# Performance work log

Hardware: AMD Instinct MI355X
Metric: run time of the kernel (lower is better)

Reference implementation:

```python
import jax, jax.numpy as jnp
import numpy as np

FP8_MAX = 448.0  # max normal of float8_e4m3fn
NUM_HEADS = 16


def act_quant(x):
    # per-tensor fp8 quantization: scale so max|x| maps to FP8_MAX
    scale = jnp.max(jnp.abs(x)) / FP8_MAX
    q = (x / scale).astype(jnp.float8_e4m3fn)
    return q, scale


def setup_inputs() -> dict:
    key = jax.random.key(0)
    k1, k2, k3, k4 = jax.random.split(key, 4)
    B, S, H = 2, 2048, 2048
    x = jax.random.normal(k1, (B, S, H), dtype=jnp.float32)
    W_qkv = jax.random.normal(k2, (H, 3 * H), dtype=jnp.float32) * (1.0 / np.sqrt(H))
    W_out = jax.random.normal(k3, (H, H), dtype=jnp.float32) * (1.0 / np.sqrt(H))
    b_out = jnp.zeros((H,), dtype=jnp.float32)
    return {"x": x, "W_qkv": W_qkv, "W_out": W_out, "b_out": b_out}


def reference(x, W_qkv, W_out, b_out):
    B, S, H = x.shape
    nH = NUM_HEADS
    hd = H // nH  # 128, matches head_dim default used for scaling

    qkv = jnp.einsum('bsh,hf->bsf', x, W_qkv)          # [B,S,3H]
    qkv = qkv.reshape(B, S, 3, nH, hd)
    q = qkv[:, :, 0].transpose(0, 2, 1, 3)             # [B,nH,S,hd]
    k = qkv[:, :, 1].transpose(0, 2, 1, 3)
    v = qkv[:, :, 2].transpose(0, 2, 1, 3)

    q8, q_scale = act_quant(q)
    k8, k_scale = act_quant(k)
    # fp8_gemm_optimized: dequantized GEMM = (a @ b) * a_scale * b_scale
    scores = jnp.einsum('bhqd,bhkd->bhqk',
                        q8.astype(jnp.float32), k8.astype(jnp.float32))
    scores = scores * (q_scale * k_scale) / jnp.sqrt(jnp.float32(hd))

    attn = jax.nn.softmax(scores, axis=-1)             # [B,nH,S,S]
    # (dropout omitted: deterministic / eval mode)

    v8, v_scale = act_quant(v)
    out = jnp.einsum('bhqk,bhkd->bhqd', attn, v8.astype(jnp.float32))
    out = out * v_scale                                # a_scale = 1 for attn weights

    out = out.transpose(0, 2, 1, 3).reshape(B, S, H)
    return jnp.einsum('bsh,ho->bso', out, W_out) + b_out
```

## Files before the change

kernel.cpp:

```cpp
#include <hip/hip_runtime.h>
#include <hip/hip_bf16.h>
#include <math.h>

#define B_   2
#define S_   2048
#define H_   2048
#define NH   16
#define HD   128
#define ROWS (B_ * S_)
#define F3   (3 * H_)
#define KS   2048
#define NKC  192

typedef _Float16 f16x8 __attribute__((ext_vector_type(8)));
typedef float    f32x4  __attribute__((ext_vector_type(4)));
typedef float    f32x16 __attribute__((ext_vector_type(16)));

union H2 { unsigned u; _Float16 h[2]; };
union H4 { ushort4 s4; _Float16 h[4]; };
union PU { unsigned u[4]; f16x8 v8; };

struct FragSet { f16x8 a[4]; f16x8 b[4]; };

__device__ __forceinline__ void gl_lds16(const void* g, void* l) {
  __builtin_amdgcn_global_load_lds(
      (const __attribute__((address_space(1))) void*)g,
      (__attribute__((address_space(3))) void*)l, 16, 0, 0);
}

__device__ __forceinline__ float quant_e4m3(float x) {
  float ax = fabsf(x);
  float q;
  if (ax < 0.015625f) {
    q = rintf(ax * 512.0f) * (1.0f / 512.0f);
  } else {
    unsigned eb = __float_as_uint(ax) & 0x7f800000u;
    float quantum = __uint_as_float(eb - (3u << 23));
    q = rintf(ax / quantum) * quantum;
    if (q > 448.0f) q = 448.0f;
  }
  return copysignf(q, x);
}

__global__ __launch_bounds__(256) void split_ab(
    const float* __restrict__ in, _Float16* __restrict__ hi,
    _Float16* __restrict__ lo) {
  const size_t i = (size_t)blockIdx.x * 256 + threadIdx.x;
  float4 v = ((const float4*)in)[i];
  H4 h, l;
  h.h[0] = (_Float16)v.x; l.h[0] = (_Float16)(v.x - (float)h.h[0]);
  h.h[1] = (_Float16)v.y; l.h[1] = (_Float16)(v.y - (float)h.h[1]);
  h.h[2] = (_Float16)v.z; l.h[2] = (_Float16)(v.z - (float)h.h[2]);
  h.h[3] = (_Float16)v.w; l.h[3] = (_Float16)(v.w - (float)h.h[3]);
  ((ushort4*)hi)[i] = h.s4;
  ((ushort4*)lo)[i] = l.s4;
}

__global__ __launch_bounds__(256) void split_tr(
    const float* __restrict__ in, _Float16* __restrict__ hi,
    _Float16* __restrict__ lo, int K, int N) {
  __shared__ _Float16 ht[64][72];
  __shared__ _Float16 lt[64][72];
  const int t = threadIdx.x;
  const int n0 = blockIdx.x * 64, k0 = blockIdx.y * 64;
#pragma unroll
  for (int p = 0; p < 4; p++) {
    const int k = p * 16 + (t >> 4);
    const int n = (t & 15) * 4;
    float4 v = *(const float4*)(in + (size_t)(k0 + k) * N + n0 + n);
    _Float16 h0 = (_Float16)v.x, h1 = (_Float16)v.y,
             h2 = (_Float16)v.z, h3 = (_Float16)v.w;
    ht[n + 0][k] = h0; lt[n + 0][k] = (_Float16)(v.x - (float)h0);
    ht[n + 1][k] = h1; lt[n + 1][k] = (_Float16)(v.y - (float)h1);
    ht[n + 2][k] = h2; lt[n + 2][k] = (_Float16)(v.z - (float)h2);
    ht[n + 3][k] = h3; lt[n + 3][k] = (_Float16)(v.w - (float)h3);
  }
  __syncthreads();
#pragma unroll
  for (int it = 0; it < 2; it++) {
    const int idx = it * 256 + t;
    const int r = idx >> 3, c = (idx & 7) * 8;
    *(uint4*)(hi + (size_t)(n0 + r) * K + k0 + c) = *(const uint4*)&ht[r][c];
    *(uint4*)(lo + (size_t)(n0 + r) * K + k0 + c) = *(const uint4*)&lt[r][c];
  }
}

#define ABUF(i) (lds + (i) * 12288)

#define STAGE32(tt, dstA) do {                                                 \
    const _Float16* As_ = ((tt) < 128) ? Ahi : Alo;                            \
    const _Float16* Bs_ = ((((tt) >> 6)) == 1) ? Btlo : Bthi;                  \
    const int koff_ = ((tt) & 63) << 5;                                        \
    {                                                                          \
      const int c0_ = t, r0_ = c0_ >> 2, cl0_ = c0_ & 3;                       \
      gl_lds16(As_ + (size_t)(row0 + r0_) * KS + koff_ + ((cl0_ ^ (r0_ & 3)) << 3), \
               (dstA) + c0_ * 8);                                              \
      const int c1_ = 512 + t, r1_ = c1_ >> 2, cl1_ = c1_ & 3;                 \
      gl_lds16(As_ + (size_t)(row0 + r1_) * KS + koff_ + ((cl1_ ^ (r1_ & 3)) << 3), \
               (dstA) + c1_ * 8);                                              \
      const int cb_ = t, rb_ = cb_ >> 2, clb_ = cb_ & 3;                       \
      gl_lds16(Bs_ + (size_t)(col0 + rb_) * KS + koff_ + ((clb_ ^ (rb_ & 3)) << 3), \
               (dstA) + 8192 + cb_ * 8);                                       \
    }                                                                          \
  } while (0)

#define READ_FRAGS(bi, FR) do {                                                \
    const _Float16* Ab_ = ABUF(bi);                                            \
    const _Float16* Bb_ = Ab_ + 8192;                                          \
    _Pragma("unroll")                                                          \
    for (int i_ = 0; i_ < 4; i_++) {                                           \
      const int r_ = wm * 64 + i_ * 16 + l15;                                  \
      (FR).a[i_] = *(const f16x8*)(Ab_ + r_ * 32 + ((g ^ (r_ & 3)) << 3));     \
    }                                                                          \
    _Pragma("unroll")                                                          \
    for (int j_ = 0; j_ < 4; j_++) {                                           \
      const int r_ = wn * 64 + j_ * 16 + l15;                                  \
      (FR).b[j_] = *(const f16x8*)(Bb_ + r_ * 32 + ((g ^ (r_ & 3)) << 3));     \
    }                                                                          \
  } while (0)

#define MFMA16(FR) do {                                                        \
    _Pragma("unroll")                                                          \
    for (int i_ = 0; i_ < 4; i_++)                                             \
      _Pragma("unroll")                                                        \
      for (int j_ = 0; j_ < 4; j_++)                                           \
        acc[i_][j_] = __builtin_amdgcn_mfma_f32_16x16x32_f16(                  \
            (FR).a[i_], (FR).b[j_], acc[i_][j_], 0, 0, 0);                     \
  } while (0)

#define BODY(u, kcv, FRc, FRn) do {                                            \
    const int kc_ = (kcv);                                                     \
    if (kc_ + 3 < NKC) STAGE32(kc_ + 3, ABUF(((u) + 3) & 3));                  \
    if (kc_ + 1 < NKC) READ_FRAGS(((u) + 1) & 3, FRn);                         \
    MFMA16(FRc);                                                               \
    if (kc_ < NKC - 3) { asm volatile("s_waitcnt vmcnt(3)" ::: "memory"); }    \
    else               { asm volatile("s_waitcnt vmcnt(0)" ::: "memory"); }    \
    __builtin_amdgcn_s_barrier();                                              \
  } while (0)

__global__ __launch_bounds__(512, 2) void gemm_split256(
    const _Float16* __restrict__ Ahi, const _Float16* __restrict__ Alo,
    const _Float16* __restrict__ Bthi, const _Float16* __restrict__ Btlo,
    float* __restrict__ C, const float* __restrict__ bias,
    unsigned* mx, int N, int has_bias) {
  __shared__ __align__(16) _Float16 lds[49152];
  const int t = threadIdx.x;
  const int wave = t >> 6, lane = t & 63;
  const int l15 = lane & 15, g = lane >> 4;
  const int wm = wave >> 1, wn = wave & 1;

  const int gx = gridDim.x;
  const int nwg = gx * gridDim.y;
  const int bid = blockIdx.y * gx + blockIdx.x;
  const int tile = (bid & 7) * (nwg >> 3) + (bid >> 3);
  const int row0 = (tile / gx) * 256, col0 = (tile % gx) * 128;

  f32x4 acc[4][4] = {};
  FragSet fr0, fr1;

  STAGE32(0, ABUF(0));
  STAGE32(1, ABUF(1));
  STAGE32(2, ABUF(2));
  asm volatile("s_waitcnt vmcnt(3)" ::: "memory");
  __builtin_amdgcn_s_barrier();
  READ_FRAGS(0, fr0);

  for (int grp = 0; grp < NKC / 4; grp++) {
    const int base = grp * 4;
    BODY(0, base + 0, fr0, fr1);
    BODY(1, base + 1, fr1, fr0);
    BODY(2, base + 2, fr0, fr1);
    BODY(3, base + 3, fr1, fr0);
  }

  float bmax = 0.0f;
#pragma unroll
  for (int j = 0; j < 4; j++) {
    const int col = col0 + wn * 64 + j * 16 + l15;
    const float bv = has_bias ? bias[col] : 0.0f;
#pragma unroll
    for (int i = 0; i < 4; i++) {
      const int rbase = row0 + wm * 64 + i * 16 + g * 4;
#pragma unroll
      for (int r = 0; r < 4; r++) {
        const float v = acc[i][j][r] + bv;
        C[(size_t)(rbase + r) * N + col] = v;
        bmax = fmaxf(bmax, fabsf(v));
      }
    }
  }

  if (mx) {
    __syncthreads();
    float* red = (float*)lds;
    red[t] = bmax;
    __syncthreads();
    for (int s2 = 256; s2 > 0; s2 >>= 1) {
      if (t < s2) red[t] = fmaxf(red[t], red[t + s2]);
      __syncthreads();
    }
    if (t == 0) atomicMax(mx + (col0 >> 11), __float_as_uint(red[0]));
  }
}

__global__ __launch_bounds__(256) void quant_qkv(
    const float* __restrict__ qkv, const unsigned* __restrict__ mx,
    _Float16* __restrict__ q8, _Float16* __restrict__ k8,
    _Float16* __restrict__ v8t) {
  __shared__ _Float16 tile[64 * 72];
  const int t = threadIdx.x;
  const int bid = blockIdx.x;

  if (bid < 16384) {
    const size_t base = ((size_t)bid * 256 + t) * 4;
    const int row = (int)(base >> 12);
    const int col = (int)(base & 4095);
    const int seg = col >> 11;
    const int c2 = col & 2047;
    const int h = c2 >> 7, d = c2 & 127;
    const int b = row >> 11, s = row & 2047;
    const float scale = __uint_as_float(mx[seg]) / 448.0f;
    float4 v = *(const float4*)(qkv + (size_t)row * F3 + col);
    H4 r;
    r.h[0] = (_Float16)quant_e4m3(v.x / scale);
    r.h[1] = (_Float16)quant_e4m3(v.y / scale);
    r.h[2] = (_Float16)quant_e4m3(v.z / scale);
    r.h[3] = (_Float16)quant_e4m3(v.w / scale);
    _Float16* dst = seg ? k8 : q8;
    const size_t di = ((size_t)((b * NH + h) * S_) + s) * HD + d;
    *(ushort4*)(dst + di) = r.s4;
  } else {
    const int bt = bid - 16384;
    const int dtile = bt & 1;
    const int stile = (bt >> 1) & 31;
    const int bh = bt >> 6;
    const int b = bh >> 4, h = bh & 15;
    const int s0 = stile * 64, d0 = dtile * 64;
    const float scale = __uint_as_float(mx[2]) / 448.0f;

#pragma unroll
    for (int r = 0; r < 4; r++) {
      const int s = s0 + r * 16 + (t >> 4);
      const int dl = (t & 15) * 4;
      float4 v = *(const float4*)(qkv + (size_t)(b * S_ + s) * F3 + 4096 + h * HD + d0 + dl);
      tile[(dl + 0) * 72 + r * 16 + (t >> 4)] = (_Float16)quant_e4m3(v.x / scale);
      tile[(dl + 1) * 72 + r * 16 + (t >> 4)] = (_Float16)quant_e4m3(v.y / scale);
      tile[(dl + 2) * 72 + r * 16 + (t >> 4)] = (_Float16)quant_e4m3(v.z / scale);
      tile[(dl + 3) * 72 + r * 16 + (t >> 4)] = (_Float16)quant_e4m3(v.w / scale);
    }
    __syncthreads();
#pragma unroll
    for (int j = 0; j < 2; j++) {
      const int wi = j * 256 + t;
      const int dl = wi >> 3;
      const int sch = (wi & 7) * 8;
      uint4 val = *(const uint4*)(tile + dl * 72 + sch);
      *(uint4*)(v8t + (size_t)bh * (HD * S_) + (size_t)(d0 + dl) * S_ + s0 + sch) = val;
    }
  }
}

__global__ __launch_bounds__(256, 2) void attn_kernel(
    const _Float16* __restrict__ q8, const _Float16* __restrict__ k8,
    const _Float16* __restrict__ v8t, const unsigned* __restrict__ mx,
    _Float16* __restrict__ oHi, _Float16* __restrict__ oLo) {
  __shared__ __align__(16) char ldsb[65536];

  const int t = threadIdx.x;
  const int wave = t >> 6;
  const int lane = t & 63;
  const int l31 = lane & 31;
  const int hf = lane >> 5;

  const int qt = blockIdx.x & 15;
  const int bh = blockIdx.x >> 4;
  const int b = bh >> 4, h = bh & 15;
  const int q0 = qt * 128 + wave * 32;

  const float qs = __uint_as_float(mx[0]) * (1.0f / 448.0f);
  const float ks = __uint_as_float(mx[1]) * (1.0f / 448.0f);
  const float vs = __uint_as_float(mx[2]) * (1.0f / 448.0f);
  const float sfac = qs * ks * 0.08838834764831843f;

  f16x8 qf[8];
  {
    const _Float16* qp = q8 + ((size_t)(bh * S_) + q0 + l31) * HD + hf * 8;
#pragma unroll
    for (int st = 0; st < 8; st++)
      qf[st] = *(const f16x8*)(qp + st * 16);
  }

  f32x16 acc[4] = {};
  float m_base = 0.0f;
  float l_run = 0.0f;

  const size_t kB_ = (size_t)(bh * S_) * HD;
  const size_t vB_ = (size_t)bh * (HD * S_);
  const int k_key = t >> 4;
  const int k_dch = (t & 15) * 8;
  const int k_wch = (((t & 15) ^ (k_key & 7)) << 3);
  const int v_d   = t >> 3;
  const int v_sch = (t & 7) * 8;
  const int v_wch = (((t & 7) ^ (v_d & 7)) << 3);

  const int NT = S_ / 64;
  uint4 kp[4], vp[4];

#pragma unroll
  for (int r = 0; r < 4; r++)
    kp[r] = *(const uint4*)(k8 + kB_ + (size_t)(r * 16 + k_key) * HD + k_dch);
#pragma unroll
  for (int r = 0; r < 4; r++)
    vp[r] = *(const uint4*)(v8t + vB_ + (size_t)(r * 32 + v_d) * S_ + v_sch);
  {
    _Float16* K0 = (_Float16*)ldsb;
    _Float16* V0 = (_Float16*)(ldsb + 32768);
#pragma unroll
    for (int r = 0; r < 4; r++)
      *(uint4*)(K0 + (r * 16 + k_key) * 128 + k_wch) = kp[r];
#pragma unroll
    for (int r = 0; r < 4; r++)
      *(uint4*)(V0 + (r * 32 + v_d) * 64 + v_wch) = vp[r];
  }
#pragma unroll
  for (int r = 0; r < 4; r++)
    kp[r] = *(const uint4*)(k8 + kB_ + (size_t)(64 + r * 16 + k_key) * HD + k_dch);
#pragma unroll
  for (int r = 0; r < 4; r++)
    vp[r] = *(const uint4*)(v8t + vB_ + (size_t)(r * 32 + v_d) * S_ + 64 + v_sch);
  __syncthreads();

  for (int kt = 0; kt < NT; kt++) {
    const _Float16* Klds  = (const _Float16*)(ldsb + (kt & 1) * 16384);
    const _Float16* VTlds = (const _Float16*)(ldsb + 32768 + (kt & 1) * 16384);
    if (kt + 1 < NT) {
      _Float16* Kn = (_Float16*)(ldsb + ((kt + 1) & 1) * 16384);
      _Float16* Vn = (_Float16*)(ldsb + 32768 + ((kt + 1) & 1) * 16384);
#pragma unroll
      for (int r = 0; r < 4; r++)
        *(uint4*)(Kn + (r * 16 + k_key) * 128 + k_wch) = kp[r];
#pragma unroll
      for (int r = 0; r < 4; r++)
        *(uint4*)(Vn + (r * 32 + v_d) * 64 + v_wch) = vp[r];
    }
    if (kt + 2 < NT) {
      const int nk = (kt + 2) * 64;
#pragma unroll
      for (int r = 0; r < 4; r++)
        kp[r] = *(const uint4*)(k8 + kB_ + (size_t)(nk + r * 16 + k_key) * HD + k_dch);
#pragma unroll
      for (int r = 0; r < 4; r++)
        vp[r] = *(const uint4*)(v8t + vB_ + (size_t)(r * 32 + v_d) * S_ + nk + v_sch);
    }

#pragma unroll
    for (int sub = 0; sub < 2; sub++) {
      const int ksub = sub * 32;
      f32x16 s = {};
      __builtin_amdgcn_s_setprio(1);
#pragma unroll
      for (int st = 0; st < 8; st++) {
        const int krow = ksub + l31;
        f16x8 af = *(const f16x8*)(Klds + krow * 128 +
                                   (((st * 2 + hf) ^ (krow & 7)) << 3));
        s = __builtin_amdgcn_mfma_f32_32x32x16_f16(af, qf[st], s, 0, 0, 0);
      }
      __builtin_amdgcn_s_setprio(0);
      f16x8 vf0 = *(const f16x8*)(VTlds + l31 * 64 +
                                  (((sub * 4 + 0 * 2 + hf) ^ (l31 & 7)) << 3));
      f16x8 vf1 = *(const f16x8*)(VTlds + l31 * 64 +
                                  (((sub * 4 + 1 * 2 + hf) ^ (l31 & 7)) << 3));
      float p[16];
      if (kt == 0 && sub == 0) {
        float tmax = -3.0e38f;
#pragma unroll
        for (int i = 0; i < 16; i++) {
          p[i] = s[i] * sfac;
          tmax = fmaxf(tmax, p[i]);
        }
        tmax = fmaxf(tmax, __shfl_xor(tmax, 32));
        m_base = tmax;
        float rs = 0.0f;
#pragma unroll
        for (int i = 0; i < 16; i++) {
          p[i] = __expf(p[i] - tmax);
          rs += p[i];
        }
        l_run += rs;
      } else {
        const float mb = m_base;
        float rs = 0.0f;
#pragma unroll
        for (int i = 0; i < 16; i++) {
          p[i] = fminf(__expf(fmaf(s[i], sfac, -mb)), 60000.0f);
          rs += p[i];
        }
        l_run += rs;
      }
      f16x8 pf[2];
#pragma unroll
      for (int c = 0; c < 2; c++) {
        const int c8 = c * 8;
        const int sidx = hf ? 0 : 4;
        const int oidx = hf ? 4 : 0;
        H2 s0h, s1h, o0h, o1h;
        s0h.h[0] = (_Float16)p[c8 + sidx];     s0h.h[1] = (_Float16)p[c8 + sidx + 1];
        s1h.h[0] = (_Float16)p[c8 + sidx + 2]; s1h.h[1] = (_Float16)p[c8 + sidx + 3];
        o0h.h[0] = (_Float16)p[c8 + oidx];     o0h.h[1] = (_Float16)p[c8 + oidx + 1];
        o1h.h[0] = (_Float16)p[c8 + oidx + 2]; o1h.h[1] = (_Float16)p[c8 + oidx + 3];
        unsigned r0 = (unsigned)__shfl_xor((int)s0h.u, 32);
        unsigned r1 = (unsigned)__shfl_xor((int)s1h.u, 32);
        PU pu;
        if (hf == 0) { pu.u[0] = o0h.u; pu.u[1] = o1h.u; pu.u[2] = r0; pu.u[3] = r1; }
        else         { pu.u[0] = r0;    pu.u[1] = r1;    pu.u[2] = o0h.u; pu.u[3] = o1h.u; }
        pf[c] = pu.v8;
      }
#pragma unroll
      for (int dt = 0; dt < 4; dt++) {
        f16x8 nf0, nf1;
        if (dt < 3) {
          const int vrow = (dt + 1) * 32 + l31;
          nf0 = *(const f16x8*)(VTlds + vrow * 64 +
                                (((sub * 4 + 0 * 2 + hf) ^ (vrow & 7)) << 3));
          nf1 = *(const f16x8*)(VTlds + vrow * 64 +
                                (((sub * 4 + 1 * 2 + hf) ^ (vrow & 7)) << 3));
        }
        __builtin_amdgcn_s_setprio(1);
        acc[dt] = __builtin_amdgcn_mfma_f32_32x32x16_f16(vf0, pf[0], acc[dt], 0, 0, 0);
        acc[dt] = __builtin_amdgcn_mfma_f32_32x32x16_f16(vf1, pf[1], acc[dt], 0, 0, 0);
        __builtin_amdgcn_s_setprio(0);
        vf0 = nf0; vf1 = nf1;
      }
    }
    __syncthreads();
  }

  l_run += __shfl_xor(l_run, 32);

  float* scr = (float*)ldsb + wave * 1056;
  const float f = vs / l_run;
#pragma unroll
  for (int dt = 0; dt < 4; dt++) {
#pragma unroll
    for (int i = 0; i < 16; i++) {
      const int dl = (i & 3) + 8 * (i >> 2) + 4 * hf;
      scr[dl * 33 + l31] = acc[dt][i] * f;
    }
    __syncthreads();
#pragma unroll
    for (int g = 0; g < 4; g++) {
      const int idx = g * 64 + lane;
      const int ql = idx >> 3;
      const int dd = (idx & 7) * 4;
      float4 o;
      o.x = scr[(dd + 0) * 33 + ql];
      o.y = scr[(dd + 1) * 33 + ql];
      o.z = scr[(dd + 2) * 33 + ql];
      o.w = scr[(dd + 3) * 33 + ql];
      H4 hh, ll;
      hh.h[0] = (_Float16)o.x; ll.h[0] = (_Float16)(o.x - (float)hh.h[0]);
      hh.h[1] = (_Float16)o.y; ll.h[1] = (_Float16)(o.y - (float)hh.h[1]);
      hh.h[2] = (_Float16)o.z; ll.h[2] = (_Float16)(o.z - (float)hh.h[2]);
      hh.h[3] = (_Float16)o.w; ll.h[3] = (_Float16)(o.w - (float)hh.h[3]);
      const int qg = q0 + ql;
      const size_t ofs = (size_t)(b * S_ + qg) * H_ + h * HD + dt * 32 + dd;
      *(ushort4*)(oHi + ofs) = hh.s4;
      *(ushort4*)(oLo + ofs) = ll.s4;
    }
    __syncthreads();
  }
}

extern "C" void kernel_launch(void* const* d_in, const int* in_sizes, int n_in,
                              void* d_out, int out_size, void* d_ws, size_t ws_size,
                              hipStream_t stream) {
  const float* x     = (const float*)d_in[0];
  const float* W_qkv = (const float*)d_in[1];
  const float* W_out = (const float*)d_in[2];
  const float* b_out = (const float*)d_in[3];
  float* out = (float*)d_out;

  char* ws = (char*)d_ws;
  float*    qkv    = (float*)ws;
  _Float16* A2hi   = (_Float16*)(ws + 33554432);
  _Float16* A2lo   = (_Float16*)(ws + 50331648);
  _Float16* B2thi  = (_Float16*)(ws + 67108864);
  _Float16* B2tlo  = (_Float16*)(ws + 75497472);
  _Float16* B1thi  = (_Float16*)(ws + 100663296);
  _Float16* B1tlo  = (_Float16*)(ws + 125829120);
  _Float16* q8     = (_Float16*)(ws + 100663296);
  _Float16* k8     = (_Float16*)(ws + 117440512);
  _Float16* v8t    = (_Float16*)(ws + 134217728);
  _Float16* A1hi   = (_Float16*)(ws + 150994944);
  _Float16* A1lo   = (_Float16*)(ws + 167772160);
  unsigned* mx     = (unsigned*)(ws + 184549376);

  hipMemsetAsync(mx, 0, 3 * sizeof(unsigned), stream);

  split_ab<<<(ROWS * H_) / 1024, 256, 0, stream>>>(x, A1hi, A1lo);
  split_tr<<<dim3(F3 / 64, H_ / 64), 256, 0, stream>>>(W_qkv, B1thi, B1tlo, H_, F3);

  gemm_split256<<<dim3(F3 / 128, ROWS / 256), 512, 0, stream>>>(
      A1hi, A1lo, B1thi, B1tlo, qkv, nullptr, mx, F3, 0);

  quant_qkv<<<16384 + B_ * NH * 32 * 2, 256, 0, stream>>>(qkv, mx, q8, k8, v8t);

  attn_kernel<<<B_ * NH * 16, 256, 0, stream>>>(q8, k8, v8t, mx, A2hi, A2lo);

  split_tr<<<dim3(H_ / 64, H_ / 64), 256, 0, stream>>>(W_out, B2thi, B2tlo, H_, H_);

  gemm_split256<<<dim3(H_ / 128, ROWS / 256), 512, 0, stream>>>(
      A2hi, A2lo, B2thi, B2tlo, out, b_out, nullptr, H_, 1);
}
```

Baseline: 794.7 us.

## Widen GEMM K-step to 64 with double-buffered LDS staging

The split-fp16 GEMM main loop now processes 64-wide K chunks instead of 32, doing 32 MFMAs per iteration. The four-slot LDS ring becomes two 24K-half buffers, and the XOR swizzle widens to 8 chunks. Staging is redistributed per wave with 8 rows each. This halves the number of barriers and loop iterations, aiming to cut synchronization overhead. In exchange, each iteration waits with vmcnt(0) for the next prefetch, which shortens how long global loads have to complete and may expose memory latency.

Result: no change. 809.2 us (+1.8%).

```diff
diff --git a/kernel.cpp b/kernel.cpp
--- a/kernel.cpp
+++ b/kernel.cpp
@@ -10,7 +10,6 @@
 #define ROWS (B_ * S_)
 #define F3   (3 * H_)
 #define KS   2048
-#define NKC  192
 
 typedef _Float16 f16x8 __attribute__((ext_vector_type(8)));
 typedef float    f32x4  __attribute__((ext_vector_type(4)));
@@ -20,7 +19,7 @@
 union H4 { ushort4 s4; _Float16 h[4]; };
 union PU { unsigned u[4]; f16x8 v8; };
 
-struct FragSet { f16x8 a[4]; f16x8 b[4]; };
+struct FragSet64 { f16x8 a0[4], a1[4], b0[4], b1[4]; };
 
 __device__ __forceinline__ void gl_lds16(const void* g, void* l) {
   __builtin_amdgcn_global_load_lds(
@@ -85,56 +84,68 @@
   }
 }
 
-#define ABUF(i) (lds + (i) * 12288)
-
-#define STAGE32(tt, dstA) do {                                                 \
-    const _Float16* As_ = ((tt) < 128) ? Ahi : Alo;                            \
-    const _Float16* Bs_ = ((((tt) >> 6)) == 1) ? Btlo : Bthi;                  \
-    const int koff_ = ((tt) & 63) << 5;                                        \
-    {                                                                          \
-      const int c0_ = t, r0_ = c0_ >> 2, cl0_ = c0_ & 3;                       \
-      gl_lds16(As_ + (size_t)(row0 + r0_) * KS + koff_ + ((cl0_ ^ (r0_ & 3)) << 3), \
-               (dstA) + c0_ * 8);                                              \
-      const int c1_ = 512 + t, r1_ = c1_ >> 2, cl1_ = c1_ & 3;                 \
-      gl_lds16(As_ + (size_t)(row0 + r1_) * KS + koff_ + ((cl1_ ^ (r1_ & 3)) << 3), \
-               (dstA) + c1_ * 8);                                              \
-      const int cb_ = t, rb_ = cb_ >> 2, clb_ = cb_ & 3;                       \
-      gl_lds16(Bs_ + (size_t)(col0 + rb_) * KS + koff_ + ((clb_ ^ (rb_ & 3)) << 3), \
-               (dstA) + 8192 + cb_ * 8);                                       \
-    }                                                                          \
+#define STAGE_A(tt, dst) do {                                                  \
+    const _Float16* As_ = ((tt) < 64) ? Ahi : Alo;                             \
+    const size_t so_ = (size_t)(row0 + wave * 8 + srow) * KS +                 \
+                       (((tt) & 31) << 6) + schunk;                            \
+    _Float16* db_ = (dst) + wave * 512;                                        \
+    gl_lds16(As_ + so_,                    db_);                               \
+    gl_lds16(As_ + so_ + (size_t)64 * KS,  db_ + 4096);                        \
+    gl_lds16(As_ + so_ + (size_t)128 * KS, db_ + 8192);                       \
+    gl_lds16(As_ + so_ + (size_t)192 * KS, db_ + 12288);                       \
   } while (0)
 
-#define READ_FRAGS(bi, FR) do {                                                \
-    const _Float16* Ab_ = ABUF(bi);                                            \
-    const _Float16* Bb_ = Ab_ + 8192;                                          \
+#define STAGE_B(tt, dst) do {                                                  \
+    const _Float16* Bs_ = ((((tt) >> 5)) == 1) ? Btlo : Bthi;                  \
+    const size_t so_ = (size_t)(col0 + wave * 8 + srow) * KS +                 \
+                       (((tt) & 31) << 6) + schunk;                            \
+    _Float16* db_ = (dst) + 16384 + wave * 512;                                \
+    gl_lds16(Bs_ + so_,                    db_);                               \
+    gl_lds16(Bs_ + so_ + (size_t)64 * KS,  db_ + 4096);                        \
+  } while (0)
+
+#define READ_FRAGS64(bufp, FR) do {                                            \
+    const _Float16* Ab_ = (bufp);                                              \
+    const _Float16* Bb_ = Ab_ + 16384;                                         \
     _Pragma("unroll")                                                          \
     for (int i_ = 0; i_ < 4; i_++) {                                           \
       const int r_ = wm * 64 + i_ * 16 + l15;                                  \
-      (FR).a[i_] = *(const f16x8*)(Ab_ + r_ * 32 + ((g ^ (r_ & 3)) << 3));     \
+      (FR).a0[i_] = *(const f16x8*)(Ab_ + r_ * 64 + ((g ^ (r_ & 7)) << 3));    \
+      (FR).a1[i_] = *(const f16x8*)(Ab_ + r_ * 64 + (((4 ^ g) ^ (r_ & 7)) << 3)); \
     }                                                                          \
     _Pragma("unroll")                                                          \
     for (int j_ = 0; j_ < 4; j_++) {                                           \
       const int r_ = wn * 64 + j_ * 16 + l15;                                  \
-      (FR).b[j_] = *(const f16x8*)(Bb_ + r_ * 32 + ((g ^ (r_ & 3)) << 3));     \
+      (FR).b0[j_] = *(const f16x8*)(Bb_ + r_ * 64 + ((g ^ (r_ & 7)) << 3));    \
+      (FR).b1[j_] = *(const f16x8*)(Bb_ + r_ * 64 + (((4 ^ g) ^ (r_ & 7)) << 3)); \
     }                                                                          \
   } while (0)
 
-#define MFMA16(FR) do {                                                        \
+#define MFMA32(FR) do {                                                        \
     _Pragma("unroll")                                                          \
     for (int i_ = 0; i_ < 4; i_++)                                             \
       _Pragma("unroll")                                                        \
       for (int j_ = 0; j_ < 4; j_++)                                           \
         acc[i_][j_] = __builtin_amdgcn_mfma_f32_16x16x32_f16(                  \
-            (FR).a[i_], (FR).b[j_], acc[i_][j_], 0, 0, 0);                     \
+            (FR).a0[i_], (FR).b0[j_], acc[i_][j_], 0, 0, 0);                   \
+    _Pragma("unroll")                                                          \
+    for (int i_ = 0; i_ < 4; i_++)                                             \
+      _Pragma("unroll")                                                        \
+      for (int j_ = 0; j_ < 4; j_++)                                           \
+        acc[i_][j_] = __builtin_amdgcn_mfma_f32_16x16x32_f16(                  \
+            (FR).a1[i_], (FR).b1[j_], acc[i_][j_], 0, 0, 0);                   \
   } while (0)
 
-#define BODY(u, kcv, FRc, FRn) do {                                            \
+#define BODY64(kcv, FRc, FRn) do {                                             \
     const int kc_ = (kcv);                                                     \
-    if (kc_ + 3 < NKC) STAGE32(kc_ + 3, ABUF(((u) + 3) & 3));                  \
-    if (kc_ + 1 < NKC) READ_FRAGS(((u) + 1) & 3, FRn);                         \
-    MFMA16(FRc);                                                               \
-    if (kc_ < NKC - 3) { asm volatile("s_waitcnt vmcnt(3)" ::: "memory"); }    \
-    else               { asm volatile("s_waitcnt vmcnt(0)" ::: "memory"); }    \
+    if (kc_ + 2 < 96) {                                                        \
+      _Float16* stg_ = lds + (kc_ & 1) * 24576;                                \
+      STAGE_A(kc_ + 2, stg_);                                                  \
+      STAGE_B(kc_ + 2, stg_);                                                  \
+    }                                                                          \
+    if (kc_ + 1 < 96) READ_FRAGS64(lds + ((kc_ + 1) & 1) * 24576, FRn);        \
+    MFMA32(FRc);                                                               \
+    asm volatile("s_waitcnt vmcnt(0) lgkmcnt(0)" ::: "memory");                \
     __builtin_amdgcn_s_barrier();                                              \
   } while (0)
 
@@ -155,22 +166,25 @@
   const int tile = (bid & 7) * (nwg >> 3) + (bid >> 3);
   const int row0 = (tile / gx) * 256, col0 = (tile % gx) * 128;
 
+  const int srow = lane >> 3;
+  const int schunk = ((lane & 7) ^ srow) << 3;
+
   f32x4 acc[4][4] = {};
-  FragSet fr0, fr1;
-
-  STAGE32(0, ABUF(0));
-  STAGE32(1, ABUF(1));
-  STAGE32(2, ABUF(2));
-  asm volatile("s_waitcnt vmcnt(3)" ::: "memory");
+  FragSet64 fr0, fr1;
+
+  STAGE_A(0, lds);
+  STAGE_B(0, lds);
+  STAGE_A(1, lds + 24576);
+  STAGE_B(1, lds + 24576);
+  asm volatile("s_waitcnt vmcnt(0)" ::: "memory");
   __builtin_amdgcn_s_barrier();
-  READ_FRAGS(0, fr0);
-
-  for (int grp = 0; grp < NKC / 4; grp++) {
-    const int base = grp * 4;
-    BODY(0, base + 0, fr0, fr1);
-    BODY(1, base + 1, fr1, fr0);
-    BODY(2, base + 2, fr0, fr1);
-    BODY(3, base + 3, fr1, fr0);
+  READ_FRAGS64(lds, fr0);
+  asm volatile("s_waitcnt lgkmcnt(0)" ::: "memory");
+  __builtin_amdgcn_s_barrier();
+
+  for (int kc2 = 0; kc2 < 96; kc2 += 2) {
+    BODY64(kc2 + 0, fr0, fr1);
+    BODY64(kc2 + 1, fr1, fr0);
   }
 
   float bmax = 0.0f;
```
